# Performance work log

Hardware: AMD Instinct MI355X
Metric: run time of the kernel (lower is better)

Reference implementation:

```python
import jax, jax.numpy as jnp
import numpy as np

H, KV, D = 12, 2, 128        # q heads, kv heads, head_dim
HID = 1536
B, S = 4, 2048               # equal-length packed sequences
T = B * S
EPS = 1e-6
ROPE_THETA = 10000.0


def _rms_norm(x, w):
    # RMSNorm over last dim in fp32, as in Qwen3RMSNorm
    xf = x.astype(jnp.float32)
    var = jnp.mean(xf * xf, axis=-1, keepdims=True)
    return (w * (xf * jax.lax.rsqrt(var + EPS))).astype(x.dtype)


def _apply_rope(x, cos, sin):
    # x: [T, h, D]; cos/sin: [T, D/2] -> expand over heads
    half = cos.shape[-1]
    x1, x2 = x[..., :half], x[..., half:2 * half]
    c = cos[:, None, :]
    s = sin[:, None, :]
    return jnp.concatenate([x1 * c - x2 * s, x1 * s + x2 * c], axis=-1)


def setup_inputs() -> dict:
    key = jax.random.key(0)
    ks = jax.random.split(key, 8)
    hidden_states = jax.random.normal(ks[0], (T, HID), dtype=jnp.float32)
    # real RoPE tables over per-sequence positions
    inv_freq = 1.0 / (ROPE_THETA ** (np.arange(0, D, 2, dtype=np.float32) / D))  # [D/2]
    pos = np.tile(np.arange(S, dtype=np.float32), B)                              # [T]
    ang = pos[:, None] * inv_freq[None, :]
    cos = jnp.asarray(np.cos(ang), dtype=jnp.float32)
    sin = jnp.asarray(np.sin(ang), dtype=jnp.float32)
    sc = 0.02
    Wq = jax.random.normal(ks[1], (HID, H * D), dtype=jnp.float32) * sc
    Wk = jax.random.normal(ks[2], (HID, KV * D), dtype=jnp.float32) * sc
    Wv = jax.random.normal(ks[3], (HID, KV * D), dtype=jnp.float32) * sc
    Wo = jax.random.normal(ks[4], (H * D, HID), dtype=jnp.float32) * sc
    q_norm_w = jnp.ones((D,), dtype=jnp.float32)
    k_norm_w = jnp.ones((D,), dtype=jnp.float32)
    cu_seqlens = jnp.arange(B + 1, dtype=jnp.int32) * S
    return {"hidden_states": hidden_states, "cos": cos, "sin": sin,
            "Wq": Wq, "Wk": Wk, "Wv": Wv, "Wo": Wo,
            "q_norm_w": q_norm_w, "k_norm_w": k_norm_w,
            "cu_seqlens": cu_seqlens}


def reference(hidden_states, cos, sin, Wq, Wk, Wv, Wo, q_norm_w, k_norm_w, cu_seqlens):
    # QKV projections on packed tokens
    q = (hidden_states @ Wq).reshape(T, H, D)
    k = (hidden_states @ Wk).reshape(T, KV, D)
    v = (hidden_states @ Wv).reshape(T, KV, D)
    # Qwen3 per-head QK RMSNorm, then RoPE
    q = _apply_rope(_rms_norm(q, q_norm_w), cos, sin)
    k = _apply_rope(_rms_norm(k, k_norm_w), cos, sin)
    # equal-length sequences: unpack to [B, h, S, D] (block-diagonal varlen attn)
    qb = q.reshape(B, S, H, D).transpose(0, 2, 1, 3)
    kb = k.reshape(B, S, KV, D).transpose(0, 2, 1, 3)
    vb = v.reshape(B, S, KV, D).transpose(0, 2, 1, 3)
    # GQA: repeat kv heads
    rep = H // KV
    kb = jnp.repeat(kb, rep, axis=1)
    vb = jnp.repeat(vb, rep, axis=1)
    scale = D ** -0.5
    scores = jnp.einsum('bhqd,bhkd->bhqk', qb, kb) * scale
    causal = jnp.tril(jnp.ones((S, S), dtype=bool))
    scores = jnp.where(causal[None, None], scores, jnp.finfo(scores.dtype).min)
    attn = jax.nn.softmax(scores, axis=-1)
    out = jnp.einsum('bhqk,bhkd->bhqd', attn, vb)       # [B,H,S,D]
    out = out.transpose(0, 2, 1, 3).reshape(T, H * D)   # repack
    return out @ Wo
```

## Files before the change

kernel.cpp:

```cpp
#include <hip/hip_runtime.h>
#include <hip/hip_bf16.h>
#include <stdint.h>

#define H_   12
#define KV_  2
#define D_   128
#define HID_ 1536
#define B_   4
#define S_   2048
#define T_   (B_*S_)

typedef __attribute__((ext_vector_type(8))) short  bf16x8;
typedef __attribute__((ext_vector_type(4))) float  f32x4;

__device__ __forceinline__ ushort f2bf(float f) {
  union { float f; uint32_t u; } v; v.f = f;
  uint32_t u = v.u;
  return (ushort)((u + 0x7fffu + ((u >> 16) & 1u)) >> 16);
}
__device__ __forceinline__ float bf2f(ushort u) {
  union { uint32_t u; float f; } v; v.u = ((uint32_t)u) << 16;
  return v.f;
}
__device__ __forceinline__ uint32_t cvtpk_bf16(float lo, float hi) {
  uint32_t r;
  asm("v_cvt_pk_bf16_f32 %0, %1, %2" : "=v"(r) : "v"(lo), "v"(hi));
  return r;
}

__device__ __forceinline__ void gload_lds16(const void* g, void* l) {
  __builtin_amdgcn_global_load_lds(
      (const __attribute__((address_space(1))) uint32_t*)g,
      (__attribute__((address_space(3))) uint32_t*)l, 16, 0, 0);
}

__global__ __launch_bounds__(256) void cvt_f32_bf16(const float* __restrict__ in,
                                                    ushort* __restrict__ out, int n) {
  int i = (blockIdx.x * 256 + threadIdx.x) * 4;
  if (i + 3 < n) {
    float4 v = *(const float4*)&in[i];
    ushort4 o;
    o.x = f2bf(v.x); o.y = f2bf(v.y); o.z = f2bf(v.z); o.w = f2bf(v.w);
    *(ushort4*)&out[i] = o;
  }
}

__global__ __launch_bounds__(256) void transpose_cvt(const float* __restrict__ W,
                                                     ushort* __restrict__ Wt,
                                                     int K, int N) {
  __shared__ float tile[32][33];
  int k0 = blockIdx.x * 32, n0 = blockIdx.y * 32;
  int tx = threadIdx.x & 31, ty = threadIdx.x >> 5;
#pragma unroll
  for (int i = 0; i < 32; i += 8)
    tile[ty + i][tx] = W[(long)(k0 + ty + i) * N + n0 + tx];
  __syncthreads();
#pragma unroll
  for (int i = 0; i < 32; i += 8)
    Wt[(long)(n0 + ty + i) * K + k0 + tx] = f2bf(tile[tx][ty + i]);
}

template <int OUT_F32>
__global__ __launch_bounds__(256, 2) void gemm_bt(const ushort* __restrict__ A,
                                                  const ushort* __restrict__ Bt,
                                                  void* __restrict__ Cv,
                                                  int M, int N, int K, int lda) {
  __shared__ ushort lA[128 * 32];
  __shared__ ushort lB[128 * 32];
  const int tid = threadIdx.x;
  const int lane = tid & 63, w = tid >> 6;
  const int wr = w >> 1, wc = w & 1;
  const int l15 = lane & 15, lh = lane >> 4;
  const long m0 = (long)blockIdx.x * 128, n0 = (long)blockIdx.y * 128;
  const ushort* Ab = A + m0 * lda;
  const ushort* Bb = Bt + n0 * K;
  const int sr = tid >> 2;
  const int sc = (tid & 3) * 8;
  const int ldsoff = w * 512;
  f32x4 acc[4][4] = {};

  for (int k0 = 0; k0 < K; k0 += 32) {
#pragma unroll
    for (int it = 0; it < 2; ++it) {
      gload_lds16(Ab + (long)(it * 64 + sr) * lda + k0 + sc, &lA[it * 2048 + ldsoff]);
      gload_lds16(Bb + (long)(it * 64 + sr) * K + k0 + sc, &lB[it * 2048 + ldsoff]);
    }
    __syncthreads();
    bf16x8 af[4], bfr[4];
    const int ra = (wr * 64 + l15) * 32 + lh * 8;
    const int rb = (wc * 64 + l15) * 32 + lh * 8;
#pragma unroll
    for (int i = 0; i < 4; ++i) {
      af[i]  = *(const bf16x8*)&lA[ra + i * 16 * 32];
      bfr[i] = *(const bf16x8*)&lB[rb + i * 16 * 32];
    }
#pragma unroll
    for (int i = 0; i < 4; ++i)
#pragma unroll
      for (int j = 0; j < 4; ++j)
        acc[i][j] = __builtin_amdgcn_mfma_f32_16x16x32_bf16(af[i], bfr[j], acc[i][j], 0, 0, 0);
    __syncthreads();
  }
#pragma unroll
  for (int i = 0; i < 4; ++i) {
#pragma unroll
    for (int q = 0; q < 4; ++q) {
      long row = m0 + wr * 64 + i * 16 + lh * 4 + q;
#pragma unroll
      for (int j = 0; j < 4; ++j) {
        long col = n0 + wc * 64 + j * 16 + l15;
        float v = acc[i][j][q];
        if (OUT_F32) ((float*)Cv)[row * N + col] = v;
        else         ((ushort*)Cv)[row * N + col] = f2bf(v);
      }
    }
  }
}

template <int NH>
__global__ __launch_bounds__(256) void normrope(const ushort* __restrict__ X,
                                                int xstride,
                                                const float* __restrict__ w,
                                                const float* __restrict__ cosb,
                                                const float* __restrict__ sinb,
                                                ushort* __restrict__ Y,
                                                float scale) {
  int wid = (int)((blockIdx.x * 256 + threadIdx.x) >> 6);
  int lane = threadIdx.x & 63;
  if (wid >= T_ * NH) return;
  int t = wid / NH, h = wid % NH;
  const ushort* xr = X + (long)t * xstride + h * 128;
  float x1 = bf2f(xr[lane]);
  float x2 = bf2f(xr[lane + 64]);
  float ss = x1 * x1 + x2 * x2;
#pragma unroll
  for (int off = 32; off; off >>= 1) ss += __shfl_xor(ss, off);
  float r = rsqrtf(ss * (1.0f / 128.0f) + 1e-6f);
  float y1 = x1 * r * w[lane] * scale;
  float y2 = x2 * r * w[lane + 64] * scale;
  float c = cosb[(long)t * 64 + lane], s = sinb[(long)t * 64 + lane];
  float o1 = y1 * c - y2 * s;
  float o2 = y1 * s + y2 * c;
  int b = t / S_, sq = t % S_;
  ushort* yr = Y + ((long)(b * NH + h) * S_ + sq) * 128;
  yr[lane]      = f2bf(o1);
  yr[lane + 64] = f2bf(o2);
}

__global__ __launch_bounds__(256) void vtrans(const ushort* __restrict__ V, int vstride, int voff,
                                              ushort* __restrict__ Vt) {
  __shared__ ushort tile[32][33];
  int s0 = blockIdx.x * 32, d0 = blockIdx.y * 32;
  int bk = blockIdx.z;
  int b = bk / KV_, g = bk % KV_;
  int tx = threadIdx.x & 31, ty = threadIdx.x >> 5;
#pragma unroll
  for (int i = 0; i < 32; i += 8)
    tile[ty + i][tx] = V[(long)(b * S_ + s0 + ty + i) * vstride + voff + g * 128 + d0 + tx];
  __syncthreads();
#pragma unroll
  for (int i = 0; i < 32; i += 8)
    Vt[(long)(bk * 128 + d0 + ty + i) * S_ + s0 + tx] = tile[tx][ty + i];
}

__global__ __launch_bounds__(256, 2) void attn(ushort* __restrict__ QKV,
                                               const ushort* __restrict__ Ka,
                                               const ushort* __restrict__ Vt,
                                               const float* __restrict__ qnw,
                                               const float* __restrict__ cosb,
                                               const float* __restrict__ sinb) {
  __shared__ ushort lK[64 * 128];
  __shared__ ushort lV[128 * 64];
  __shared__ ushort lP[4 * 32 * 32];
  const int tid = threadIdx.x, lane = tid & 63, w = tid >> 6;
  const int l15 = lane & 15, lh = lane >> 4;
  char* cK = (char*)lK;
  char* cV = (char*)lV;
  char* cP = (char*)lP + w * 2048;
  const int swzK = l15 << 4;
  const int swzV = (l15 & 7) << 4;
  const int swzP = (l15 & 3) << 4;
  const float SCL = 0.08838834764831845f * 1.44269504088896f;
  const float M0  = 17.0f;

  const int qt = 15 - (int)(blockIdx.x / 48);
  const int bh = blockIdx.x % 48;
  const int b = bh / H_, h = bh % H_, g = h / (H_ / KV_);
  const int q0 = qt * 128;
  const ushort* Kb = Ka + (long)(b * KV_ + g) * S_ * 128;
  const ushort* Vb = Vt + (long)(b * KV_ + g) * 128 * S_;

  bf16x8 qf[2][4];
#pragma unroll
  for (int m = 0; m < 2; ++m) {
    const long tt = (long)b * S_ + q0 + w * 32 + m * 16 + l15;
    const ushort* xr = QKV + tt * 2048 + h * 128;
    bf16x8 raw[4];
#pragma unroll
    for (int kd = 0; kd < 4; ++kd)
      raw[kd] = *(const bf16x8*)&xr[kd * 32 + lh * 8];
    float ss = 0.f;
#pragma unroll
    for (int kd = 0; kd < 4; ++kd)
#pragma unroll
      for (int e = 0; e < 8; ++e) {
        float v = bf2f((ushort)raw[kd][e]);
        ss += v * v;
      }
    ss += __shfl_xor(ss, 16);
    ss += __shfl_xor(ss, 32);
    const float rn = rsqrtf(ss * (1.0f / 128.0f) + 1e-6f) * SCL;
    const float* cR = cosb + tt * 64;
    const float* sR = sinb + tt * 64;
#pragma unroll
    for (int kp = 0; kp < 2; ++kp) {
      bf16x8 qlo, qhi;
#pragma unroll
      for (int e = 0; e < 8; ++e) {
        const int ci = kp * 32 + lh * 8 + e;
        float c = cR[ci], s = sR[ci];
        float y1 = bf2f((ushort)raw[kp][e])     * rn * qnw[ci];
        float y2 = bf2f((ushort)raw[kp + 2][e]) * rn * qnw[64 + ci];
        qlo[e] = (short)f2bf(y1 * c - y2 * s);
        qhi[e] = (short)f2bf(y1 * s + y2 * c);
      }
      qf[m][kp]     = qlo;
      qf[m][kp + 2] = qhi;
    }
  }

  f32x4 o[2][8] = {};
  float lr[2] = {0.f, 0.f};
  const int nt = 2 * qt + 2;

  bf16x8 kreg[4], vreg[4];
#define LDTILE(K0) do { \
  _Pragma("unroll") for (int it = 0; it < 4; ++it) \
    kreg[it] = *(const bf16x8*)&Kb[(long)((K0) + it * 16 + (tid >> 4)) * 128 + (tid & 15) * 8]; \
  _Pragma("unroll") for (int it = 0; it < 4; ++it) \
    vreg[it] = *(const bf16x8*)&Vb[(long)(it * 32 + (tid >> 3)) * S_ + (K0) + (tid & 7) * 8]; \
} while (0)

  LDTILE(0);
  for (int t = 0; t < nt; ++t) {
    const int k0 = t * 64;
    __syncthreads();
#pragma unroll
    for (int it = 0; it < 4; ++it) {
      int r = it * 16 + (tid >> 4);
      *(bf16x8*)(cK + r * 256 + (((tid & 15) * 16) ^ (((tid >> 4) & 15) << 4))) = kreg[it];
    }
#pragma unroll
    for (int it = 0; it < 4; ++it) {
      int r = it * 32 + (tid >> 3);
      *(bf16x8*)(cV + r * 128 + (((tid & 7) * 16) ^ ((r & 7) << 4))) = vreg[it];
    }
    __syncthreads();
    if (t + 1 < nt) LDTILE(k0 + 64);

    if (k0 <= q0 + w * 32 + 31) {
      f32x4 sfr[2][4] = {};
      __builtin_amdgcn_s_setprio(1);
#pragma unroll
      for (int kd = 0; kd < 4; ++kd) {
        bf16x8 kf[4];
#pragma unroll
        for (int n = 0; n < 4; ++n)
          kf[n] = *(const bf16x8*)(cK + (n * 16 + l15) * 256 + ((kd * 64 + lh * 16) ^ swzK));
#pragma unroll
        for (int m = 0; m < 2; ++m)
#pragma unroll
          for (int n = 0; n < 4; ++n)
            sfr[m][n] = __builtin_amdgcn_mfma_f32_16x16x32_bf16(kf[n], qf[m][kd], sfr[m][n], 0, 0, 0);
      }
      __builtin_amdgcn_s_setprio(0);
      const bool boundary = (k0 + 63 > q0 + w * 32);
      if (boundary) {
#pragma unroll
        for (int m = 0; m < 2; ++m) {
          const int rowm = q0 + w * 32 + m * 16 + l15;
#pragma unroll
          for (int n = 0; n < 4; ++n) {
            int kb = k0 + n * 16 + lh * 4;
#pragma unroll
            for (int qr = 0; qr < 4; ++qr)
              if (kb + qr > rowm) sfr[m][n][qr] = -INFINITY;
          }
        }
      }
#pragma unroll
      for (int m = 0; m < 2; ++m) {
#pragma unroll
        for (int n = 0; n < 4; ++n) {
          float p0 = exp2f(sfr[m][n][0] - M0);
          float p1 = exp2f(sfr[m][n][1] - M0);
          float p2 = exp2f(sfr[m][n][2] - M0);
          float p3 = exp2f(sfr[m][n][3] - M0);
          sfr[m][n][0] = p0; sfr[m][n][1] = p1; sfr[m][n][2] = p2; sfr[m][n][3] = p3;
          lr[m] += (p0 + p1) + (p2 + p3);
        }
      }
#pragma unroll
      for (int kf2 = 0; kf2 < 2; ++kf2) {
#pragma unroll
        for (int m = 0; m < 2; ++m)
#pragma unroll
          for (int nl = 0; nl < 2; ++nl) {
            const int n = kf2 * 2 + nl;
            uint2 pk;
            pk.x = cvtpk_bf16(sfr[m][n][0], sfr[m][n][1]);
            pk.y = cvtpk_bf16(sfr[m][n][2], sfr[m][n][3]);
            *(uint2*)(cP + (m * 16 + l15) * 64 + ((nl * 32 + lh * 8) ^ swzP)) = pk;
          }
        const int cb = (lh * 16) ^ swzP;
        bf16x8 pf0 = *(const bf16x8*)(cP + l15 * 64 + cb);
        bf16x8 pf1 = *(const bf16x8*)(cP + (16 + l15) * 64 + cb);
        const int cv = (kf2 * 64 + lh * 16);
        __builtin_amdgcn_s_setprio(1);
#pragma unroll
        for (int dblk = 0; dblk < 8; ++dblk) {
          bf16x8 vf = *(const bf16x8*)(cV + (dblk * 16 + l15) * 128 + (cv ^ swzV));
          o[0][dblk] = __builtin_amdgcn_mfma_f32_16x16x32_bf16(pf0, vf, o[0][dblk], 0, 0, 0);
          o[1][dblk] = __builtin_amdgcn_mfma_f32_16x16x32_bf16(pf1, vf, o[1][dblk], 0, 0, 0);
        }
        __builtin_amdgcn_s_setprio(0);
      }
    }
  }
#undef LDTILE
#pragma unroll
  for (int m = 0; m < 2; ++m) {
    lr[m] += __shfl_xor(lr[m], 16);
    lr[m] += __shfl_xor(lr[m], 32);
    float inv = 1.f / lr[m];
#pragma unroll
    for (int qr = 0; qr < 4; ++qr) {
      float iv = __shfl(inv, lh * 4 + qr);
      long trow = (long)b * S_ + q0 + w * 32 + m * 16 + lh * 4 + qr;
#pragma unroll
      for (int dblk = 0; dblk < 8; ++dblk)
        QKV[trow * 2048 + h * 128 + dblk * 16 + l15] = f2bf(o[m][dblk][qr] * iv);
    }
  }
}

extern "C" void kernel_launch(void* const* d_in, const int* in_sizes, int n_in,
                              void* d_out, int out_size, void* d_ws, size_t ws_size,
                              hipStream_t stream) {
  const float* hs   = (const float*)d_in[0];
  const float* cosb = (const float*)d_in[1];
  const float* sinb = (const float*)d_in[2];
  const float* Wq   = (const float*)d_in[3];
  const float* Wk   = (const float*)d_in[4];
  const float* Wv   = (const float*)d_in[5];
  const float* Wo   = (const float*)d_in[6];
  const float* qw   = (const float*)d_in[7];
  const float* kw   = (const float*)d_in[8];
  (void)in_sizes; (void)n_in; (void)out_size; (void)ws_size;

  char* ws = (char*)d_ws;
  size_t off = 0;
  auto alloc = [&](size_t bytes) {
    void* p = ws + off;
    off += (bytes + 255) & ~(size_t)255;
    return p;
  };
  ushort* Xb  = (ushort*)alloc((size_t)T_ * HID_ * 2);
  ushort* Wqt = (ushort*)alloc((size_t)HID_ * HID_ * 2);
  ushort* Wkt = (ushort*)alloc((size_t)256 * HID_ * 2);
  ushort* Wvt = (ushort*)alloc((size_t)256 * HID_ * 2);
  ushort* Wot = (ushort*)alloc((size_t)HID_ * HID_ * 2);
  ushort* qkv = (ushort*)alloc((size_t)T_ * 2048 * 2);
  ushort* ka  = (ushort*)alloc((size_t)T_ * 256 * 2);
  ushort* vt  = (ushort*)alloc((size_t)T_ * 256 * 2);

  cvt_f32_bf16<<<(T_ * HID_ / 4 + 255) / 256, 256, 0, stream>>>(hs, Xb, T_ * HID_);
  transpose_cvt<<<dim3(HID_ / 32, HID_ / 32), 256, 0, stream>>>(Wq, Wqt, HID_, HID_);
  transpose_cvt<<<dim3(HID_ / 32, 256 / 32), 256, 0, stream>>>(Wk, Wkt, HID_, 256);
  transpose_cvt<<<dim3(HID_ / 32, 256 / 32), 256, 0, stream>>>(Wv, Wvt, HID_, 256);
  transpose_cvt<<<dim3(HID_ / 32, HID_ / 32), 256, 0, stream>>>(Wo, Wot, HID_, HID_);

  gemm_bt<0><<<dim3(T_ / 128, 2048 / 128), 256, 0, stream>>>(Xb, Wqt, qkv, T_, 2048, HID_, HID_);

  normrope<KV_><<<(T_ * KV_ + 3) / 4, 256, 0, stream>>>(qkv + 1536, 2048, kw, cosb, sinb, ka, 1.0f);
  vtrans<<<dim3(S_ / 32, 128 / 32, B_ * KV_), 256, 0, stream>>>(qkv, 2048, 1792, vt);

  attn<<<768, 256, 0, stream>>>(qkv, ka, vt, qw, cosb, sinb);

  gemm_bt<1><<<dim3(T_ / 128, 1536 / 128), 256, 0, stream>>>(qkv, Wot, (float*)d_out, T_, 1536, HID_, 2048);
}
```

Baseline: 232.7 us.

## Pair short and long causal query blocks per workgroup for load balance

The attention kernel now handles 64-row query blocks, one 16-row slice per wave, and each workgroup processes a mirrored pair (p and 31-p) of causal blocks in sequence, so every workgroup does roughly equal KV work. Previously each block took a 128-row tile and blocks were ordered longest-first. This evens out tail imbalance and halves per-wave register state (one m-tile), which may help occupancy. In exchange, K/V tiles are reloaded per query block with half the reuse per load, and each wave issues fewer MFMAs per LDS fragment read.

```diff
diff --git a/kernel.cpp b/kernel.cpp
--- a/kernel.cpp
+++ b/kernel.cpp
@@ -171,67 +171,23 @@
                                                const float* __restrict__ sinb) {
   __shared__ ushort lK[64 * 128];
   __shared__ ushort lV[128 * 64];
-  __shared__ ushort lP[4 * 32 * 32];
+  __shared__ ushort lP[4 * 16 * 32];
   const int tid = threadIdx.x, lane = tid & 63, w = tid >> 6;
   const int l15 = lane & 15, lh = lane >> 4;
   char* cK = (char*)lK;
   char* cV = (char*)lV;
-  char* cP = (char*)lP + w * 2048;
+  char* cP = (char*)lP + w * 1024;
   const int swzK = l15 << 4;
   const int swzV = (l15 & 7) << 4;
   const int swzP = (l15 & 3) << 4;
   const float SCL = 0.08838834764831845f * 1.44269504088896f;
   const float M0  = 17.0f;
 
-  const int qt = 15 - (int)(blockIdx.x / 48);
+  const int p  = (int)(blockIdx.x / 48);
   const int bh = blockIdx.x % 48;
   const int b = bh / H_, h = bh % H_, g = h / (H_ / KV_);
-  const int q0 = qt * 128;
   const ushort* Kb = Ka + (long)(b * KV_ + g) * S_ * 128;
   const ushort* Vb = Vt + (long)(b * KV_ + g) * 128 * S_;
-
-  bf16x8 qf[2][4];
-#pragma unroll
-  for (int m = 0; m < 2; ++m) {
-    const long tt = (long)b * S_ + q0 + w * 32 + m * 16 + l15;
-    const ushort* xr = QKV + tt * 2048 + h * 128;
-    bf16x8 raw[4];
-#pragma unroll
-    for (int kd = 0; kd < 4; ++kd)
-      raw[kd] = *(const bf16x8*)&xr[kd * 32 + lh * 8];
-    float ss = 0.f;
-#pragma unroll
-    for (int kd = 0; kd < 4; ++kd)
-#pragma unroll
-      for (int e = 0; e < 8; ++e) {
-        float v = bf2f((ushort)raw[kd][e]);
-        ss += v * v;
-      }
-    ss += __shfl_xor(ss, 16);
-    ss += __shfl_xor(ss, 32);
-    const float rn = rsqrtf(ss * (1.0f / 128.0f) + 1e-6f) * SCL;
-    const float* cR = cosb + tt * 64;
-    const float* sR = sinb + tt * 64;
-#pragma unroll
-    for (int kp = 0; kp < 2; ++kp) {
-      bf16x8 qlo, qhi;
-#pragma unroll
-      for (int e = 0; e < 8; ++e) {
-        const int ci = kp * 32 + lh * 8 + e;
-        float c = cR[ci], s = sR[ci];
-        float y1 = bf2f((ushort)raw[kp][e])     * rn * qnw[ci];
-        float y2 = bf2f((ushort)raw[kp + 2][e]) * rn * qnw[64 + ci];
-        qlo[e] = (short)f2bf(y1 * c - y2 * s);
-        qhi[e] = (short)f2bf(y1 * s + y2 * c);
-      }
-      qf[m][kp]     = qlo;
-      qf[m][kp + 2] = qhi;
-    }
-  }
-
-  f32x4 o[2][8] = {};
-  float lr[2] = {0.f, 0.f};
-  const int nt = 2 * qt + 2;
 
   bf16x8 kreg[4], vreg[4];
 #define LDTILE(K0) do { \
@@ -241,107 +197,139 @@
     vreg[it] = *(const bf16x8*)&Vb[(long)(it * 32 + (tid >> 3)) * S_ + (K0) + (tid & 7) * 8]; \
 } while (0)
 
-  LDTILE(0);
-  for (int t = 0; t < nt; ++t) {
-    const int k0 = t * 64;
-    __syncthreads();
-#pragma unroll
-    for (int it = 0; it < 4; ++it) {
-      int r = it * 16 + (tid >> 4);
-      *(bf16x8*)(cK + r * 256 + (((tid & 15) * 16) ^ (((tid >> 4) & 15) << 4))) = kreg[it];
-    }
-#pragma unroll
-    for (int it = 0; it < 4; ++it) {
-      int r = it * 32 + (tid >> 3);
-      *(bf16x8*)(cV + r * 128 + (((tid & 7) * 16) ^ ((r & 7) << 4))) = vreg[it];
-    }
-    __syncthreads();
-    if (t + 1 < nt) LDTILE(k0 + 64);
-
-    if (k0 <= q0 + w * 32 + 31) {
-      f32x4 sfr[2][4] = {};
-      __builtin_amdgcn_s_setprio(1);
-#pragma unroll
-      for (int kd = 0; kd < 4; ++kd) {
-        bf16x8 kf[4];
-#pragma unroll
-        for (int n = 0; n < 4; ++n)
-          kf[n] = *(const bf16x8*)(cK + (n * 16 + l15) * 256 + ((kd * 64 + lh * 16) ^ swzK));
-#pragma unroll
-        for (int m = 0; m < 2; ++m)
+  for (int half = 0; half < 2; ++half) {
+    const int qblk = half ? (31 - p) : p;
+    const int q0 = qblk * 64;
+    const int nt = qblk + 1;
+
+    bf16x8 qf[4];
+    {
+      const long tt = (long)b * S_ + q0 + w * 16 + l15;
+      const ushort* xr = QKV + tt * 2048 + h * 128;
+      bf16x8 raw[4];
+#pragma unroll
+      for (int kd = 0; kd < 4; ++kd)
+        raw[kd] = *(const bf16x8*)&xr[kd * 32 + lh * 8];
+      float ss = 0.f;
+#pragma unroll
+      for (int kd = 0; kd < 4; ++kd)
+#pragma unroll
+        for (int e = 0; e < 8; ++e) {
+          float v = bf2f((ushort)raw[kd][e]);
+          ss += v * v;
+        }
+      ss += __shfl_xor(ss, 16);
+      ss += __shfl_xor(ss, 32);
+      const float rn = rsqrtf(ss * (1.0f / 128.0f) + 1e-6f) * SCL;
+      const float* cR = cosb + tt * 64;
+      const float* sR = sinb + tt * 64;
+#pragma unroll
+      for (int kp = 0; kp < 2; ++kp) {
+        bf16x8 qlo, qhi;
+#pragma unroll
+        for (int e = 0; e < 8; ++e) {
+          const int ci = kp * 32 + lh * 8 + e;
+          float c = cR[ci], s = sR[ci];
+          float y1 = bf2f((ushort)raw[kp][e])     * rn * qnw[ci];
+          float y2 = bf2f((ushort)raw[kp + 2][e]) * rn * qnw[64 + ci];
+          qlo[e] = (short)f2bf(y1 * c - y2 * s);
+          qhi[e] = (short)f2bf(y1 * s + y2 * c);
+        }
+        qf[kp]     = qlo;
+        qf[kp + 2] = qhi;
+      }
+    }
+
+    f32x4 o[8] = {};
+    float lr = 0.f;
+
+    LDTILE(0);
+    for (int t = 0; t < nt; ++t) {
+      const int k0 = t * 64;
+      __syncthreads();
+#pragma unroll
+      for (int it = 0; it < 4; ++it) {
+        int r = it * 16 + (tid >> 4);
+        *(bf16x8*)(cK + r * 256 + (((tid & 15) * 16) ^ (((tid >> 4) & 15) << 4))) = kreg[it];
+      }
+#pragma unroll
+      for (int it = 0; it < 4; ++it) {
+        int r = it * 32 + (tid >> 3);
+        *(bf16x8*)(cV + r * 128 + (((tid & 7) * 16) ^ ((r & 7) << 4))) = vreg[it];
+      }
+      __syncthreads();
+      if (t + 1 < nt) LDTILE(k0 + 64);
+
+      if (k0 <= q0 + w * 16 + 15) {
+        f32x4 sfr[4] = {};
+        __builtin_amdgcn_s_setprio(1);
+#pragma unroll
+        for (int kd = 0; kd < 4; ++kd) {
+          bf16x8 kf[4];
 #pragma unroll
           for (int n = 0; n < 4; ++n)
-            sfr[m][n] = __builtin_amdgcn_mfma_f32_16x16x32_bf16(kf[n], qf[m][kd], sfr[m][n], 0, 0, 0);
-      }
-      __builtin_amdgcn_s_setprio(0);
-      const bool boundary = (k0 + 63 > q0 + w * 32);
-      if (boundary) {
-#pragma unroll
-        for (int m = 0; m < 2; ++m) {
-          const int rowm = q0 + w * 32 + m * 16 + l15;
+            kf[n] = *(const bf16x8*)(cK + (n * 16 + l15) * 256 + ((kd * 64 + lh * 16) ^ swzK));
+#pragma unroll
+          for (int n = 0; n < 4; ++n)
+            sfr[n] = __builtin_amdgcn_mfma_f32_16x16x32_bf16(kf[n], qf[kd], sfr[n], 0, 0, 0);
+        }
+        __builtin_amdgcn_s_setprio(0);
+        const bool boundary = (k0 + 63 > q0 + w * 16);
+        if (boundary) {
+          const int rowm = q0 + w * 16 + l15;
 #pragma unroll
           for (int n = 0; n < 4; ++n) {
             int kb = k0 + n * 16 + lh * 4;
 #pragma unroll
             for (int qr = 0; qr < 4; ++qr)
-              if (kb + qr > rowm) sfr[m][n][qr] = -INFINITY;
+              if (kb + qr > rowm) sfr[n][qr] = -INFINITY;
           }
         }
-      }
-#pragma unroll
-      for (int m = 0; m < 2; ++m) {
 #pragma unroll
         for (int n = 0; n < 4; ++n) {
-          float p0 = exp2f(sfr[m][n][0] - M0);
-          float p1 = exp2f(sfr[m][n][1] - M0);
-          float p2 = exp2f(sfr[m][n][2] - M0);
-          float p3 = exp2f(sfr[m][n][3] - M0);
-          sfr[m][n][0] = p0; sfr[m][n][1] = p1; sfr[m][n][2] = p2; sfr[m][n][3] = p3;
-          lr[m] += (p0 + p1) + (p2 + p3);
-        }
-      }
-#pragma unroll
-      for (int kf2 = 0; kf2 < 2; ++kf2) {
-#pragma unroll
-        for (int m = 0; m < 2; ++m)
+          float p0 = exp2f(sfr[n][0] - M0);
+          float p1 = exp2f(sfr[n][1] - M0);
+          float p2 = exp2f(sfr[n][2] - M0);
+          float p3 = exp2f(sfr[n][3] - M0);
+          sfr[n][0] = p0; sfr[n][1] = p1; sfr[n][2] = p2; sfr[n][3] = p3;
+          lr += (p0 + p1) + (p2 + p3);
+        }
+#pragma unroll
+        for (int kf2 = 0; kf2 < 2; ++kf2) {
 #pragma unroll
           for (int nl = 0; nl < 2; ++nl) {
             const int n = kf2 * 2 + nl;
             uint2 pk;
-            pk.x = cvtpk_bf16(sfr[m][n][0], sfr[m][n][1]);
-            pk.y = cvtpk_bf16(sfr[m][n][2], sfr[m][n][3]);
-            *(uint2*)(cP + (m * 16 + l15) * 64 + ((nl * 32 + lh * 8) ^ swzP)) = pk;
+            pk.x = cvtpk_bf16(sfr[n][0], sfr[n][1]);
+            pk.y = cvtpk_bf16(sfr[n][2], sfr[n][3]);
+            *(uint2*)(cP + l15 * 64 + ((nl * 32 + lh * 8) ^ swzP)) = pk;
           }
-        const int cb = (lh * 16) ^ swzP;
-        bf16x8 pf0 = *(const bf16x8*)(cP + l15 * 64 + cb);
-        bf16x8 pf1 = *(const bf16x8*)(cP + (16 + l15) * 64 + cb);
-        const int cv = (kf2 * 64 + lh * 16);
-        __builtin_amdgcn_s_setprio(1);
-#pragma unroll
-        for (int dblk = 0; dblk < 8; ++dblk) {
-          bf16x8 vf = *(const bf16x8*)(cV + (dblk * 16 + l15) * 128 + (cv ^ swzV));
-          o[0][dblk] = __builtin_amdgcn_mfma_f32_16x16x32_bf16(pf0, vf, o[0][dblk], 0, 0, 0);
-          o[1][dblk] = __builtin_amdgcn_mfma_f32_16x16x32_bf16(pf1, vf, o[1][dblk], 0, 0, 0);
-        }
-        __builtin_amdgcn_s_setprio(0);
-      }
+          const int cb = (lh * 16) ^ swzP;
+          bf16x8 pf = *(const bf16x8*)(cP + l15 * 64 + cb);
+          const int cv = (kf2 * 64 + lh * 16);
+          __builtin_amdgcn_s_setprio(1);
+#pragma unroll
+          for (int dblk = 0; dblk < 8; ++dblk) {
+            bf16x8 vf = *(const bf16x8*)(cV + (dblk * 16 + l15) * 128 + (cv ^ swzV));
+            o[dblk] = __builtin_amdgcn_mfma_f32_16x16x32_bf16(pf, vf, o[dblk], 0, 0, 0);
+          }
+          __builtin_amdgcn_s_setprio(0);
+        }
+      }
+    }
+    lr += __shfl_xor(lr, 16);
+    lr += __shfl_xor(lr, 32);
+    float inv = 1.f / lr;
+#pragma unroll
+    for (int qr = 0; qr < 4; ++qr) {
+      float iv = __shfl(inv, lh * 4 + qr);
+      long trow = (long)b * S_ + q0 + w * 16 + lh * 4 + qr;
+#pragma unroll
+      for (int dblk = 0; dblk < 8; ++dblk)
+        QKV[trow * 2048 + h * 128 + dblk * 16 + l15] = f2bf(o[dblk][qr] * iv);
     }
   }
 #undef LDTILE
-#pragma unroll
-  for (int m = 0; m < 2; ++m) {
-    lr[m] += __shfl_xor(lr[m], 16);
-    lr[m] += __shfl_xor(lr[m], 32);
-    float inv = 1.f / lr[m];
-#pragma unroll
-    for (int qr = 0; qr < 4; ++qr) {
-      float iv = __shfl(inv, lh * 4 + qr);
-      long trow = (long)b * S_ + q0 + w * 32 + m * 16 + lh * 4 + qr;
-#pragma unroll
-      for (int dblk = 0; dblk < 8; ++dblk)
-        QKV[trow * 2048 + h * 128 + dblk * 16 + l15] = f2bf(o[m][dblk][qr] * iv);
-    }
-  }
 }
 
 extern "C" void kernel_launch(void* const* d_in, const int* in_sizes, int n_in,
```

Measured after the change: 251.7 us. 1.08x slower.
